# Performance work log

Hardware: AMD Instinct MI355X
Metric: run time of the kernel (lower is better)

Reference implementation:

```python
import jax, jax.numpy as jnp
import numpy as np

B = 4096      # batch (tokens)
D_IN = 1024   # input_size_expert
D_HID = 4096  # hidden_size_expert
D_OUT = 1024  # output_size
E = 8         # num_experts


def setup_inputs() -> dict:
    key = jax.random.key(0)
    ks = jax.random.split(key, 9)
    s = lambda fan_in: 1.0 / np.sqrt(fan_in)
    x_expert = jax.random.normal(ks[0], (B, D_IN), dtype=jnp.float32)
    # per-expert weights stacked on leading E axis
    W1 = jax.random.uniform(ks[1], (E, D_IN, D_HID), jnp.float32, -s(D_IN), s(D_IN))
    b1 = jax.random.uniform(ks[2], (E, D_HID), jnp.float32, -s(D_IN), s(D_IN))
    W2 = jax.random.uniform(ks[3], (E, D_HID, D_OUT), jnp.float32, -s(D_HID), s(D_HID))
    b2 = jax.random.uniform(ks[4], (E, D_OUT), jnp.float32, -s(D_HID), s(D_HID))
    # gating network (input_size_gating = input_size_expert, hidden_size_gating = hidden_size_expert)
    Wg1 = jax.random.uniform(ks[5], (D_IN, D_HID), jnp.float32, -s(D_IN), s(D_IN))
    bg1 = jax.random.uniform(ks[6], (D_HID,), jnp.float32, -s(D_IN), s(D_IN))
    Wg2 = jax.random.uniform(ks[7], (D_HID, E), jnp.float32, -s(D_HID), s(D_HID))
    bg2 = jax.random.uniform(ks[8], (E,), jnp.float32, -s(D_HID), s(D_HID))
    return {"x_expert": x_expert, "W1": W1, "b1": b1, "W2": W2, "b2": b2,
            "Wg1": Wg1, "bg1": bg1, "Wg2": Wg2, "bg2": bg2}


def reference(x_expert, W1, b1, W2, b2, Wg1, bg1, Wg2, bg2):
    # gating: MLP + softmax over experts -> [B, E]
    g = jax.nn.relu(x_expert @ Wg1 + bg1)
    gate = jax.nn.softmax(g @ Wg2 + bg2, axis=1)
    # all experts as one batched GEMM: [B, E, D_HID]
    h = jax.nn.relu(jnp.einsum('bi,eih->beh', x_expert, W1) + b1)
    expert_out = jnp.einsum('beh,eho->beo', h, W2) + b2  # [B, E, D_OUT]
    # gate-weighted sum over experts
    return jnp.einsum('be,beo->bo', gate, expert_out)
```

## Files before the change

kernel.cpp:

```cpp
#include <hip/hip_runtime.h>
#include <stdint.h>

typedef __bf16 bf16;
typedef __attribute__((ext_vector_type(8))) __bf16 bf16x8;
typedef __attribute__((ext_vector_type(4))) float f32x4;
typedef unsigned short u16;
typedef unsigned int u32;

#define B_TOK 4096
#define D_IN  1024
#define D_HID 4096
#define D_OUT 1024
#define NE    8
#define KTOT  (NE * D_HID)

__device__ __forceinline__ u16 f2bf(float f) {
  u32 u = __float_as_uint(f);
  return (u16)((u + 0x7FFFu + ((u >> 16) & 1u)) >> 16);
}
__device__ __forceinline__ u32 pack2(float a, float b) {
  return (u32)f2bf(a) | ((u32)f2bf(b) << 16);
}

__global__ __launch_bounds__(256) void cvt_bf16_kernel(const float* __restrict__ in,
                                                       u32* __restrict__ out, long n) {
  long i = ((long)blockIdx.x * 256 + threadIdx.x) * 8;
  if (i >= n) return;
  const float4* pf = (const float4*)(in + i);
  float4 f0 = pf[0], f1 = pf[1];
  uint4 o = make_uint4(pack2(f0.x, f0.y), pack2(f0.z, f0.w),
                       pack2(f1.x, f1.y), pack2(f1.z, f1.w));
  *(uint4*)(out + i / 2) = o;
}

__global__ __launch_bounds__(256) void transpose_bf16_kernel(const float* __restrict__ in,
                                                             u16* __restrict__ out,
                                                             int R, int C) {
  __shared__ float tile[32][33];
  const size_t bo = (size_t)blockIdx.z * R * C;
  const int c0 = blockIdx.x * 32, r0 = blockIdx.y * 32;
  const int tx = threadIdx.x & 31, ty = threadIdx.x >> 5;
#pragma unroll
  for (int i = 0; i < 32; i += 8)
    tile[ty + i][tx] = in[bo + (size_t)(r0 + ty + i) * C + c0 + tx];
  __syncthreads();
#pragma unroll
  for (int i = 0; i < 32; i += 8)
    out[bo + (size_t)(c0 + ty + i) * R + r0 + tx] = f2bf(tile[tx][ty + i]);
}

template<int MODE>
__global__ __launch_bounds__(256, 4) void gemm_mfma(
    const bf16* __restrict__ A,
    const bf16* __restrict__ Bt,
    const float* __restrict__ bias,
    const float* __restrict__ gate,
    void* __restrict__ Cptr,
    int K, long ldB, long kOffB, long ldC, int kIters, int eArg)
{
  __shared__ __align__(16) bf16 smem[2 * 128 * 32];
  bf16* As = smem;
  bf16* Bs = smem + 128 * 32;

  const int tid  = threadIdx.x;
  const int wave = tid >> 6;
  const int lane = tid & 63;
  const int quad = lane >> 4;
  const int l16  = lane & 15;

  const int m0 = blockIdx.x * 128;
  const int n0 = blockIdx.y * 128;

  int expert = 0;
  long cColOff = 0;
  const bf16* Bp = Bt;
  const float* biasP = bias;
  if (MODE == 1) {
    if (gridDim.z > 1) { expert = blockIdx.z; cColOff = (long)expert * D_HID; }
    else               { expert = eArg; }
    Bp = Bt + (size_t)expert * D_HID * (size_t)ldB;
    biasP = bias + (size_t)expert * D_HID;
  }
  const long kBase = (MODE == 2) ? (long)blockIdx.z * kIters * 32 : 0;

  const int sRow = lane >> 2;
  const int sCol = (lane & 3) * 8;

  f32x4 acc[4][4];
#pragma unroll
  for (int i = 0; i < 4; ++i)
#pragma unroll
    for (int j = 0; j < 4; ++j)
      acc[i][j] = (f32x4){0.f, 0.f, 0.f, 0.f};

  const int wr = (wave >> 1) * 64;
  const int wc = (wave & 1) * 64;

  const bf16* aBase = A  + (size_t)(m0 + wave * 32 + sRow) * K   + kBase + sCol;
  const bf16* bBase = Bp + (size_t)(n0 + wave * 32 + sRow) * ldB + kOffB + kBase + sCol;
  bf16* asDst = As + (wave * 32) * 32;
  bf16* bsDst = Bs + (wave * 32) * 32;

  for (int kk = 0; kk < kIters; ++kk) {
    const long ko = (long)kk * 32;
#pragma unroll
    for (int s = 0; s < 2; ++s) {
      __builtin_amdgcn_global_load_lds(
          (__attribute__((address_space(1))) void*)(aBase + (size_t)(s * 16) * K + ko),
          (__attribute__((address_space(3))) void*)(asDst + s * 16 * 32), 16, 0, 0);
      __builtin_amdgcn_global_load_lds(
          (__attribute__((address_space(1))) void*)(bBase + (size_t)(s * 16) * ldB + ko),
          (__attribute__((address_space(3))) void*)(bsDst + s * 16 * 32), 16, 0, 0);
    }
    __syncthreads();
    bf16x8 af[4], bfv[4];
#pragma unroll
    for (int i = 0; i < 4; ++i) {
      af[i]  = *(const bf16x8*)(As + (wr + i * 16 + l16) * 32 + quad * 8);
      bfv[i] = *(const bf16x8*)(Bs + (wc + i * 16 + l16) * 32 + quad * 8);
    }
#pragma unroll
    for (int i = 0; i < 4; ++i)
#pragma unroll
      for (int j = 0; j < 4; ++j)
        acc[i][j] = __builtin_amdgcn_mfma_f32_16x16x32_bf16(af[i], bfv[j], acc[i][j], 0, 0, 0);
    __syncthreads();
  }

  if (MODE <= 1) {
    const int SL = 72;
    u16* slab = (u16*)smem + wave * (16 * SL);
    u16* C = (u16*)Cptr;
    float bv[4];
#pragma unroll
    for (int j = 0; j < 4; ++j) bv[j] = biasP[n0 + wc + j * 16 + l16];
#pragma unroll
    for (int i = 0; i < 4; ++i) {
#pragma unroll
      for (int r = 0; r < 4; ++r) {
        const int lrow = quad * 4 + r;
        float sc = 1.0f;
        if (MODE == 1) sc = gate[(size_t)(m0 + wr + i * 16 + lrow) * NE + expert];
#pragma unroll
        for (int j = 0; j < 4; ++j) {
          float v = fmaxf(acc[i][j][r] + bv[j], 0.0f) * sc;
          slab[lrow * SL + j * 16 + l16] = f2bf(v);
        }
      }
      const int rrow = lane & 15;
      const int c0c  = lane >> 4;
      bf16x8 v0 = *(const bf16x8*)(slab + rrow * SL + c0c * 8);
      bf16x8 v1 = *(const bf16x8*)(slab + rrow * SL + (c0c + 4) * 8);
      u16* orow = C + (size_t)(m0 + wr + i * 16 + rrow) * ldC + cColOff + n0 + wc;
      *(bf16x8*)(orow + c0c * 8)       = v0;
      *(bf16x8*)(orow + (c0c + 4) * 8) = v1;
    }
  } else {
    float* C = (float*)Cptr;
#pragma unroll
    for (int i = 0; i < 4; ++i) {
#pragma unroll
      for (int r = 0; r < 4; ++r) {
        const int row = m0 + wr + i * 16 + quad * 4 + r;
        float* crow = C + (size_t)row * ldC + n0 + wc + l16;
#pragma unroll
        for (int j = 0; j < 4; ++j)
          atomicAdd(crow + j * 16, acc[i][j][r]);
      }
    }
  }
}

__global__ __launch_bounds__(256) void gate_softmax_kernel(const bf16* __restrict__ g,
                                                           const float* __restrict__ Wg2,
                                                           const float* __restrict__ bg2,
                                                           float* __restrict__ gate) {
  const int wave = threadIdx.x >> 6, lane = threadIdx.x & 63;
  const int row = blockIdx.x * 4 + wave;
  const bf16* gr = g + (size_t)row * D_HID;
  float acc[NE];
#pragma unroll
  for (int e = 0; e < NE; ++e) acc[e] = 0.f;
  for (int k = lane; k < D_HID; k += 64) {
    const float gv = (float)gr[k];
    const float* w = Wg2 + (size_t)k * NE;
#pragma unroll
    for (int e = 0; e < NE; ++e) acc[e] += gv * w[e];
  }
#pragma unroll
  for (int e = 0; e < NE; ++e) {
    float v = acc[e];
#pragma unroll
    for (int off = 32; off > 0; off >>= 1) v += __shfl_down(v, off);
    acc[e] = v;
  }
  if (lane == 0) {
    float mx = -3.4e38f;
#pragma unroll
    for (int e = 0; e < NE; ++e) { acc[e] += bg2[e]; mx = fmaxf(mx, acc[e]); }
    float s = 0.f;
#pragma unroll
    for (int e = 0; e < NE; ++e) { acc[e] = __expf(acc[e] - mx); s += acc[e]; }
    const float inv = 1.f / s;
#pragma unroll
    for (int e = 0; e < NE; ++e) gate[(size_t)row * NE + e] = acc[e] * inv;
  }
}

__global__ __launch_bounds__(256) void gate_bias_kernel(const float* __restrict__ gate,
                                                        const float* __restrict__ b2,
                                                        float* __restrict__ out) {
  const int idx = blockIdx.x * 256 + threadIdx.x;
  const int b = idx >> 8;
  const int o = (idx & 255) * 4;
  float4 v = {0.f, 0.f, 0.f, 0.f};
#pragma unroll
  for (int e = 0; e < NE; ++e) {
    const float gv = gate[(size_t)b * NE + e];
    const float4 bb = *(const float4*)(b2 + (size_t)e * D_OUT + o);
    v.x += gv * bb.x; v.y += gv * bb.y; v.z += gv * bb.z; v.w += gv * bb.w;
  }
  *(float4*)(out + (size_t)b * D_OUT + o) = v;
}

extern "C" void kernel_launch(void* const* d_in, const int* in_sizes, int n_in,
                              void* d_out, int out_size, void* d_ws, size_t ws_size,
                              hipStream_t stream) {
  const float* x   = (const float*)d_in[0];
  const float* W1  = (const float*)d_in[1];
  const float* b1  = (const float*)d_in[2];
  const float* W2  = (const float*)d_in[3];
  const float* b2  = (const float*)d_in[4];
  const float* Wg1 = (const float*)d_in[5];
  const float* bg1 = (const float*)d_in[6];
  const float* Wg2 = (const float*)d_in[7];
  const float* bg2 = (const float*)d_in[8];
  float* out = (float*)d_out;

  char* p = (char*)d_ws;
  bf16* xb   = (bf16*)p; p += (size_t)B_TOK * D_IN * 2;
  bf16* Wg1t = (bf16*)p; p += (size_t)D_HID * D_IN * 2;
  bf16* W1t  = (bf16*)p; p += (size_t)NE * D_HID * D_IN * 2;
  bf16* W2t  = (bf16*)p; p += (size_t)D_OUT * KTOT * 2;
  bf16* g    = (bf16*)p; p += (size_t)B_TOK * D_HID * 2;
  float* gate= (float*)p; p += (size_t)B_TOK * NE * 4;
  bf16* hs   = (bf16*)p;
  const size_t fixed = (size_t)(p - (char*)d_ws);
  const bool big = ws_size >= fixed + (size_t)B_TOK * KTOT * 2;

  cvt_bf16_kernel<<<(B_TOK * D_IN / 8 + 255) / 256, 256, 0, stream>>>(x, (u32*)xb, (long)B_TOK * D_IN);
  transpose_bf16_kernel<<<dim3(D_HID / 32, D_IN / 32, 1), 256, 0, stream>>>(Wg1, (u16*)Wg1t, D_IN, D_HID);
  transpose_bf16_kernel<<<dim3(D_HID / 32, D_IN / 32, NE), 256, 0, stream>>>(W1, (u16*)W1t, D_IN, D_HID);
  transpose_bf16_kernel<<<dim3(D_OUT / 32, KTOT / 32, 1), 256, 0, stream>>>(W2, (u16*)W2t, KTOT, D_OUT);
  gemm_mfma<0><<<dim3(32, 32, 1), 256, 0, stream>>>(xb, Wg1t, bg1, nullptr, g,
                                                    D_IN, (long)D_IN, 0L, (long)D_HID, D_IN / 32, 0);
  gate_softmax_kernel<<<B_TOK / 4, 256, 0, stream>>>(g, Wg2, bg2, gate);
  gate_bias_kernel<<<B_TOK * D_OUT / 4 / 256, 256, 0, stream>>>(gate, b2, out);

  if (big) {
    gemm_mfma<1><<<dim3(32, 32, NE), 256, 0, stream>>>(xb, W1t, b1, gate, hs,
                                                       D_IN, (long)D_IN, 0L, (long)KTOT, D_IN / 32, 0);
    gemm_mfma<2><<<dim3(32, 8, 4), 256, 0, stream>>>(hs, W2t, nullptr, nullptr, out,
                                                     KTOT, (long)KTOT, 0L, (long)D_OUT, KTOT / 4 / 32, 0);
  } else {
    for (int e = 0; e < NE; ++e) {
      gemm_mfma<1><<<dim3(32, 32, 1), 256, 0, stream>>>(xb, W1t, b1, gate, hs,
                                                        D_IN, (long)D_IN, 0L, (long)D_HID, D_IN / 32, e);
      gemm_mfma<2><<<dim3(32, 8, 2), 256, 0, stream>>>(hs, W2t, nullptr, nullptr, out,
                                                       D_HID, (long)KTOT, (long)e * D_HID, (long)D_OUT,
                                                       D_HID / 2 / 32, e);
    }
  }
}
```

Baseline: 1.130 ms.

## Double GEMM K-tile to 64 with XOR-swizzled LDS and vectorize weight transpose

The GEMM K-step per LDS stage grows from 32 to 64, halving the number of loop iterations and barrier pairs. An XOR swizzle on the LDS column index is added to avoid bank conflicts on the fragment reads. The weight transpose kernel moves to 64x64 tiles with float4 loads, in-LDS bf16 conversion and 16-byte stores. LDS per block doubles to 32KB, which may limit occupancy at 4 blocks per CU.

```diff
diff --git a/kernel.cpp b/kernel.cpp
--- a/kernel.cpp
+++ b/kernel.cpp
@@ -36,17 +36,30 @@
 __global__ __launch_bounds__(256) void transpose_bf16_kernel(const float* __restrict__ in,
                                                              u16* __restrict__ out,
                                                              int R, int C) {
-  __shared__ float tile[32][33];
+  __shared__ u16 tileT[64][68];
   const size_t bo = (size_t)blockIdx.z * R * C;
-  const int c0 = blockIdx.x * 32, r0 = blockIdx.y * 32;
-  const int tx = threadIdx.x & 31, ty = threadIdx.x >> 5;
-#pragma unroll
-  for (int i = 0; i < 32; i += 8)
-    tile[ty + i][tx] = in[bo + (size_t)(r0 + ty + i) * C + c0 + tx];
+  const int c0 = blockIdx.x * 64, r0 = blockIdx.y * 64;
+  const int tid = threadIdx.x;
+  const int lr = tid >> 4;
+  const int lc = (tid & 15) * 4;
+#pragma unroll
+  for (int p = 0; p < 4; ++p) {
+    const int r = p * 16 + lr;
+    const float4 v = *(const float4*)(in + bo + (size_t)(r0 + r) * C + c0 + lc);
+    tileT[lc + 0][r] = f2bf(v.x);
+    tileT[lc + 1][r] = f2bf(v.y);
+    tileT[lc + 2][r] = f2bf(v.z);
+    tileT[lc + 3][r] = f2bf(v.w);
+  }
   __syncthreads();
-#pragma unroll
-  for (int i = 0; i < 32; i += 8)
-    out[bo + (size_t)(c0 + ty + i) * R + r0 + tx] = f2bf(tile[tx][ty + i]);
+  const int oc  = tid >> 3;
+  const int och = (tid & 7) * 8;
+#pragma unroll
+  for (int p = 0; p < 2; ++p) {
+    const int c = p * 32 + oc;
+    bf16x8 v = *(const bf16x8*)(&tileT[c][och]);
+    *(bf16x8*)(out + bo + (size_t)(c0 + c) * R + r0 + och) = v;
+  }
 }
 
 template<int MODE>
@@ -58,9 +71,9 @@
     void* __restrict__ Cptr,
     int K, long ldB, long kOffB, long ldC, int kIters, int eArg)
 {
-  __shared__ __align__(16) bf16 smem[2 * 128 * 32];
+  __shared__ __align__(16) bf16 smem[2 * 128 * 64];
   bf16* As = smem;
-  bf16* Bs = smem + 128 * 32;
+  bf16* Bs = smem + 128 * 64;
 
   const int tid  = threadIdx.x;
   const int wave = tid >> 6;
@@ -81,10 +94,10 @@
     Bp = Bt + (size_t)expert * D_HID * (size_t)ldB;
     biasP = bias + (size_t)expert * D_HID;
   }
-  const long kBase = (MODE == 2) ? (long)blockIdx.z * kIters * 32 : 0;
-
-  const int sRow = lane >> 2;
-  const int sCol = (lane & 3) * 8;
+  const long kBase = (MODE == 2) ? (long)blockIdx.z * kIters * 64 : 0;
+
+  const int sRow = lane >> 3;
+  const int sCol = ((lane & 7) ^ sRow) * 8;
 
   f32x4 acc[4][4];
 #pragma unroll
@@ -98,32 +111,36 @@
 
   const bf16* aBase = A  + (size_t)(m0 + wave * 32 + sRow) * K   + kBase + sCol;
   const bf16* bBase = Bp + (size_t)(n0 + wave * 32 + sRow) * ldB + kOffB + kBase + sCol;
-  bf16* asDst = As + (wave * 32) * 32;
-  bf16* bsDst = Bs + (wave * 32) * 32;
+  bf16* asDst = As + (wave * 32) * 64;
+  bf16* bsDst = Bs + (wave * 32) * 64;
 
   for (int kk = 0; kk < kIters; ++kk) {
-    const long ko = (long)kk * 32;
-#pragma unroll
-    for (int s = 0; s < 2; ++s) {
+    const long ko = (long)kk * 64;
+#pragma unroll
+    for (int s = 0; s < 4; ++s) {
       __builtin_amdgcn_global_load_lds(
-          (__attribute__((address_space(1))) void*)(aBase + (size_t)(s * 16) * K + ko),
-          (__attribute__((address_space(3))) void*)(asDst + s * 16 * 32), 16, 0, 0);
+          (__attribute__((address_space(1))) void*)(aBase + (size_t)(s * 8) * K + ko),
+          (__attribute__((address_space(3))) void*)(asDst + s * 8 * 64), 16, 0, 0);
       __builtin_amdgcn_global_load_lds(
-          (__attribute__((address_space(1))) void*)(bBase + (size_t)(s * 16) * ldB + ko),
-          (__attribute__((address_space(3))) void*)(bsDst + s * 16 * 32), 16, 0, 0);
+          (__attribute__((address_space(1))) void*)(bBase + (size_t)(s * 8) * ldB + ko),
+          (__attribute__((address_space(3))) void*)(bsDst + s * 8 * 64), 16, 0, 0);
     }
     __syncthreads();
-    bf16x8 af[4], bfv[4];
-#pragma unroll
-    for (int i = 0; i < 4; ++i) {
-      af[i]  = *(const bf16x8*)(As + (wr + i * 16 + l16) * 32 + quad * 8);
-      bfv[i] = *(const bf16x8*)(Bs + (wc + i * 16 + l16) * 32 + quad * 8);
-    }
-#pragma unroll
-    for (int i = 0; i < 4; ++i)
-#pragma unroll
-      for (int j = 0; j < 4; ++j)
-        acc[i][j] = __builtin_amdgcn_mfma_f32_16x16x32_bf16(af[i], bfv[j], acc[i][j], 0, 0, 0);
+#pragma unroll
+    for (int t = 0; t < 2; ++t) {
+      bf16x8 af[4], bfv[4];
+      const int sw = (((t << 2) + quad) ^ (l16 & 7)) << 3;
+#pragma unroll
+      for (int i = 0; i < 4; ++i) {
+        af[i]  = *(const bf16x8*)(As + (wr + i * 16 + l16) * 64 + sw);
+        bfv[i] = *(const bf16x8*)(Bs + (wc + i * 16 + l16) * 64 + sw);
+      }
+#pragma unroll
+      for (int i = 0; i < 4; ++i)
+#pragma unroll
+        for (int j = 0; j < 4; ++j)
+          acc[i][j] = __builtin_amdgcn_mfma_f32_16x16x32_bf16(af[i], bfv[j], acc[i][j], 0, 0, 0);
+    }
     __syncthreads();
   }
 
@@ -249,26 +266,26 @@
   const bool big = ws_size >= fixed + (size_t)B_TOK * KTOT * 2;
 
   cvt_bf16_kernel<<<(B_TOK * D_IN / 8 + 255) / 256, 256, 0, stream>>>(x, (u32*)xb, (long)B_TOK * D_IN);
-  transpose_bf16_kernel<<<dim3(D_HID / 32, D_IN / 32, 1), 256, 0, stream>>>(Wg1, (u16*)Wg1t, D_IN, D_HID);
-  transpose_bf16_kernel<<<dim3(D_HID / 32, D_IN / 32, NE), 256, 0, stream>>>(W1, (u16*)W1t, D_IN, D_HID);
-  transpose_bf16_kernel<<<dim3(D_OUT / 32, KTOT / 32, 1), 256, 0, stream>>>(W2, (u16*)W2t, KTOT, D_OUT);
+  transpose_bf16_kernel<<<dim3(D_HID / 64, D_IN / 64, 1), 256, 0, stream>>>(Wg1, (u16*)Wg1t, D_IN, D_HID);
+  transpose_bf16_kernel<<<dim3(D_HID / 64, D_IN / 64, NE), 256, 0, stream>>>(W1, (u16*)W1t, D_IN, D_HID);
+  transpose_bf16_kernel<<<dim3(D_OUT / 64, KTOT / 64, 1), 256, 0, stream>>>(W2, (u16*)W2t, KTOT, D_OUT);
   gemm_mfma<0><<<dim3(32, 32, 1), 256, 0, stream>>>(xb, Wg1t, bg1, nullptr, g,
-                                                    D_IN, (long)D_IN, 0L, (long)D_HID, D_IN / 32, 0);
+                                                    D_IN, (long)D_IN, 0L, (long)D_HID, D_IN / 64, 0);
   gate_softmax_kernel<<<B_TOK / 4, 256, 0, stream>>>(g, Wg2, bg2, gate);
   gate_bias_kernel<<<B_TOK * D_OUT / 4 / 256, 256, 0, stream>>>(gate, b2, out);
 
   if (big) {
     gemm_mfma<1><<<dim3(32, 32, NE), 256, 0, stream>>>(xb, W1t, b1, gate, hs,
-                                                       D_IN, (long)D_IN, 0L, (long)KTOT, D_IN / 32, 0);
+                                                       D_IN, (long)D_IN, 0L, (long)KTOT, D_IN / 64, 0);
     gemm_mfma<2><<<dim3(32, 8, 4), 256, 0, stream>>>(hs, W2t, nullptr, nullptr, out,
-                                                     KTOT, (long)KTOT, 0L, (long)D_OUT, KTOT / 4 / 32, 0);
+                                                     KTOT, (long)KTOT, 0L, (long)D_OUT, KTOT / 4 / 64, 0);
   } else {
     for (int e = 0; e < NE; ++e) {
       gemm_mfma<1><<<dim3(32, 32, 1), 256, 0, stream>>>(xb, W1t, b1, gate, hs,
-                                                        D_IN, (long)D_IN, 0L, (long)D_HID, D_IN / 32, e);
+                                                        D_IN, (long)D_IN, 0L, (long)D_HID, D_IN / 64, e);
       gemm_mfma<2><<<dim3(32, 8, 2), 256, 0, stream>>>(hs, W2t, nullptr, nullptr, out,
                                                        D_HID, (long)KTOT, (long)e * D_HID, (long)D_OUT,
-                                                       D_HID / 2 / 32, e);
-    }
-  }
-}
+                                                       D_HID / 2 / 64, e);
+    }
+  }
+}
```

Result: faster. 1.018 ms (-9.9%).
